# Kernel tuning notes

Measured on AMD Instinct MI355X. Metric: run time of the kernel, lower is better.

The kernel has to match this reference:

```python
import jax, jax.numpy as jnp
import numpy as np

P, V, GRID = 64, 6890, 32
V_SUB = 256          # vertex subsample for the SDF-grid proxy
SCALE_FACTOR = 0.2   # forward() default
SDF_BAND = 0.15      # proxy: phi = relu(band - dist_to_surface) >= 0
N_FACES = 13776


def _trilinear(vol, pts):
    """torch grid_sample 3D, mode=bilinear, padding=zeros, align_corners=False.
    vol: [D,H,W]; pts: [...,3] with (x,y,z) in [-1,1] mapping to (W,H,D)."""
    D, H, W = vol.shape
    x = ((pts[..., 0] + 1.0) * W - 1.0) * 0.5
    y = ((pts[..., 1] + 1.0) * H - 1.0) * 0.5
    z = ((pts[..., 2] + 1.0) * D - 1.0) * 0.5
    x0 = jnp.floor(x).astype(jnp.int32); fx = x - x0
    y0 = jnp.floor(y).astype(jnp.int32); fy = y - y0
    z0 = jnp.floor(z).astype(jnp.int32); fz = z - z0

    def corner(xi, yi, zi, w):
        inb = (xi >= 0) & (xi < W) & (yi >= 0) & (yi < H) & (zi >= 0) & (zi < D)
        v = vol[jnp.clip(zi, 0, D - 1), jnp.clip(yi, 0, H - 1), jnp.clip(xi, 0, W - 1)]
        return jnp.where(inb, v, 0.0) * w

    return (corner(x0,     y0,     z0,     (1 - fx) * (1 - fy) * (1 - fz))
          + corner(x0 + 1, y0,     z0,     fx       * (1 - fy) * (1 - fz))
          + corner(x0,     y0 + 1, z0,     (1 - fx) * fy       * (1 - fz))
          + corner(x0 + 1, y0 + 1, z0,     fx       * fy       * (1 - fz))
          + corner(x0,     y0,     z0 + 1, (1 - fx) * (1 - fy) * fz)
          + corner(x0 + 1, y0,     z0 + 1, fx       * (1 - fy) * fz)
          + corner(x0,     y0 + 1, z0 + 1, (1 - fx) * fy       * fz)
          + corner(x0 + 1, y0 + 1, z0 + 1, fx       * fy       * fz))


def _compute_phi(verts_cs):
    """Deterministic non-negative SDF-grid proxy (stands in for the external
    SDF CUDA op; original computes it under no_grad). verts_cs: [P,V,3] in [-1,1].
    Returns phi: [P,GRID,GRID,GRID] (D,H,W indexing)."""
    # cell centers in normalized coords (align_corners=False convention)
    lin = (2.0 * jnp.arange(GRID, dtype=verts_cs.dtype) + 1.0) / GRID - 1.0
    zz, yy, xx = jnp.meshgrid(lin, lin, lin, indexing='ij')
    gp = jnp.stack([xx, yy, zz], axis=-1).reshape(-1, 3)  # [G^3,3] (x,y,z)
    stride = V // V_SUB
    sub = verts_cs[:, ::stride, :][:, :V_SUB]             # [P,V_SUB,3]

    def per_person(v):  # v: [V_SUB,3]
        d2 = jnp.sum((gp[:, None, :] - v[None, :, :]) ** 2, axis=-1)  # [G^3,V_SUB]
        d = jnp.sqrt(jnp.min(d2, axis=-1))
        return jnp.maximum(SDF_BAND - d, 0.0).reshape(GRID, GRID, GRID)

    return jax.lax.map(per_person, sub)  # sequential over people: bounds peak memory


def _forward(vertices, translation):
    sg = jax.lax.stop_gradient
    verts = vertices + translation[:, None, :]                      # [P,V,3]
    n = verts.shape[0]
    bmin = sg(jnp.min(verts, axis=1))                               # [P,3] (no_grad bboxes)
    bmax = sg(jnp.max(verts, axis=1))
    # overlap(i,j) per axis: not (min_i > max_j or min_j > max_i)
    ov = jnp.all((bmin[:, None, :] <= bmax[None, :, :]) &
                 (bmin[None, :, :] <= bmax[:, None, :]), axis=-1)   # [P,P], diag True
    # faithful to original ~filter_isolated_boxes: kept only if overlapping ALL others
    valid = jnp.all(ov, axis=1)                                     # [P]
    nv = jnp.sum(valid.astype(verts.dtype))
    center = (bmin + bmax) * 0.5                                    # [P,3]
    scale = (1.0 + SCALE_FACTOR) * 0.5 * jnp.max(bmax - bmin, axis=-1)  # [P]
    verts_cs = sg((verts - center[:, None, :]) / scale[:, None, None])
    phi = sg(_compute_phi(verts_cs))                                # [P,G,G,G]
    # coordinates of ALL people's vertices in person-i's grid frame: [P,P,V,3]
    loc = (verts[None, :, :, :] - center[:, None, None, :]) / scale[:, None, None, None]
    phi_val = jax.vmap(_trilinear)(phi, loc.reshape(n, n * V, 3)).reshape(n, n, V)
    # pair (i,j) contributes iff both valid and i != j (weights[i]=0 in the loop)
    pair_w = (valid[:, None] & valid[None, :] & ~jnp.eye(n, dtype=bool)).astype(verts.dtype)
    denom = jnp.maximum(nv, 1.0) ** 2
    return jnp.sum(pair_w * jnp.sum(phi_val, axis=-1)) / denom


def setup_inputs() -> dict:
    key = jax.random.key(0)
    k1, k2, k3 = jax.random.split(key, 3)
    vertices = jax.random.normal(k1, (P, V, 3), dtype=jnp.float32) * 0.2
    translation = jax.random.uniform(k2, (P, 3), dtype=jnp.float32, minval=-0.3, maxval=0.3)
    faces = jax.random.randint(k3, (N_FACES, 3), 0, V, dtype=jnp.int32)
    return {"vertices": vertices, "translation": translation, "faces": faces}


def reference(vertices, translation, faces):
    # faces only feed the external SDF op (replaced by the phi proxy); unused here
    return _forward(vertices, translation)
```

## Files before the change

### kernel.cpp

```cpp
#include <hip/hip_runtime.h>


#define NP 64
#define NVERT 6890
#define NV3 (NVERT*3)
#define GRD 32
#define QDIM 34
#define QPLANE (QDIM*QDIM)
#define QVOL (QDIM*QPLANE)
#define VSUB 256
#define VSTRIDE 26
#define BAND 0.15f
#define PHI_SCALE 64.0f
#define INV_PHI_SCALE 0.015625f
#define LDS_BYTES (QVOL*2 + 64)
#define SAMPLE_BLOCKS (8*NP)

typedef float floatx2 __attribute__((ext_vector_type(2)));

__device__ __forceinline__ float wave_min(float v) {
  #pragma unroll
  for (int off = 32; off > 0; off >>= 1) v = fminf(v, __shfl_down(v, off));
  return v;
}
__device__ __forceinline__ float wave_max(float v) {
  #pragma unroll
  for (int off = 32; off > 0; off >>= 1) v = fmaxf(v, __shfl_down(v, off));
  return v;
}
__device__ __forceinline__ float wave_sum(float v) {
  #pragma unroll
  for (int off = 32; off > 0; off >>= 1) v += __shfl_down(v, off);
  return v;
}

__global__ __launch_bounds__(1024) void k_soa_bounds(
    const float* __restrict__ verts, const float* __restrict__ trans,
    float* __restrict__ vertsT, float* __restrict__ bbox,
    float* __restrict__ accp, unsigned int* __restrict__ donep) {
  int p = blockIdx.x;
  int tid = threadIdx.x;
  if (p == 0 && tid == 0) { accp[0] = 0.0f; donep[0] = 0u; }
  const float* vp = verts + (size_t)p * NV3;
  float tx = trans[p*3+0], ty = trans[p*3+1], tz = trans[p*3+2];
  float* o0 = vertsT + (size_t)(p*3+0) * NVERT;
  float* o1 = vertsT + (size_t)(p*3+1) * NVERT;
  float* o2 = vertsT + (size_t)(p*3+2) * NVERT;
  float mnx=1e30f, mny=1e30f, mnz=1e30f, mxx=-1e30f, mxy=-1e30f, mxz=-1e30f;
  for (int t2 = tid; t2 < NVERT/2; t2 += 1024) {
    const float* b = vp + t2*6;
    floatx2 A = *(const floatx2*)(b);
    floatx2 B = *(const floatx2*)(b+2);
    floatx2 C = *(const floatx2*)(b+4);
    mnx=fminf(mnx,fminf(A.x,B.y)); mxx=fmaxf(mxx,fmaxf(A.x,B.y));
    mny=fminf(mny,fminf(A.y,C.x)); mxy=fmaxf(mxy,fmaxf(A.y,C.x));
    mnz=fminf(mnz,fminf(B.x,C.y)); mxz=fmaxf(mxz,fmaxf(B.x,C.y));
    floatx2 sx = {A.x+tx, B.y+tx};
    floatx2 sy = {A.y+ty, C.x+ty};
    floatx2 sz = {B.x+tz, C.y+tz};
    *(floatx2*)(o0 + 2*t2) = sx;
    *(floatx2*)(o1 + 2*t2) = sy;
    *(floatx2*)(o2 + 2*t2) = sz;
  }
  mnx=wave_min(mnx)+tx; mny=wave_min(mny)+ty; mnz=wave_min(mnz)+tz;
  mxx=wave_max(mxx)+tx; mxy=wave_max(mxy)+ty; mxz=wave_max(mxz)+tz;
  __shared__ float s[16][6];
  int wave = tid >> 6, lane = tid & 63;
  if (lane == 0) {
    s[wave][0]=mnx; s[wave][1]=mny; s[wave][2]=mnz;
    s[wave][3]=mxx; s[wave][4]=mxy; s[wave][5]=mxz;
  }
  __syncthreads();
  if (tid == 0) {
    float a0=s[0][0],a1=s[0][1],a2=s[0][2],b0=s[0][3],b1=s[0][4],b2=s[0][5];
    for (int w = 1; w < 16; ++w) {
      a0=fminf(a0,s[w][0]); a1=fminf(a1,s[w][1]); a2=fminf(a2,s[w][2]);
      b0=fmaxf(b0,s[w][3]); b1=fmaxf(b1,s[w][4]); b2=fmaxf(b2,s[w][5]);
    }
    bbox[p*3+0]=a0; bbox[p*3+1]=a1; bbox[p*3+2]=a2;
    bbox[192+p*3+0]=b0; bbox[192+p*3+1]=b1; bbox[192+p*3+2]=b2;
  }
}

__global__ __launch_bounds__(1024) void k_phi(
    const float* __restrict__ verts, const float* __restrict__ trans,
    const float* __restrict__ bbox, unsigned short* __restrict__ pairs,
    float* __restrict__ centerg,
    float* __restrict__ validg, int* __restrict__ jlistg,
    int* __restrict__ jcountg, float* __restrict__ nvg) {
  int p = blockIdx.x >> 2;
  int zq = blockIdx.x & 3;
  int tid = threadIdx.x;
  int x = tid & 31, y = tid >> 5;

  __shared__ float kv[VSUB][3];
  __shared__ float phib[8][32][32];
  __shared__ int nkeep;

  const float inv = 1.0f / (float)GRD;
  if (tid == 0) nkeep = 0;
  __syncthreads();

  float bx0 = bbox[p*3+0], by0 = bbox[p*3+1], bz0 = bbox[p*3+2];
  float bx1 = bbox[192+p*3+0], by1 = bbox[192+p*3+1], bz1 = bbox[192+p*3+2];
  float cx = 0.5f*(bx0+bx1), cy = 0.5f*(by0+by1), cz = 0.5f*(bz0+bz1);
  float ext = fmaxf(bx1-bx0, fmaxf(by1-by0, bz1-bz0));
  float is = 1.0f / (0.6f * ext);

  if (zq == 0 && tid == 0) {
    centerg[p*4+0] = cx; centerg[p*4+1] = cy; centerg[p*4+2] = cz;
    centerg[p*4+3] = is * 16.0f;
  }
  if (blockIdx.x == 0 && tid < 64) {
    bool valid = true;
    for (int j = 0; j < NP; ++j) {
      bool ov = true;
      #pragma unroll
      for (int c = 0; c < 3; ++c)
        ov = ov && (bbox[tid*3+c] <= bbox[192+j*3+c]) &&
                   (bbox[j*3+c] <= bbox[192+tid*3+c]);
      valid = valid && ov;
    }
    unsigned long long mm = __ballot(valid);
    if (valid) {
      int pos = (int)__popcll(mm & ((1ull << tid) - 1ull));
      jlistg[pos] = tid;
    }
    validg[tid] = valid ? 1.0f : 0.0f;
    if (tid == 0) {
      jcountg[0] = (int)__popcll(mm);
      nvg[0] = (float)__popcll(mm);
    }
  }

  if (tid < VSUB) {
    int v = tid * VSTRIDE;
    const float* vp = verts + (size_t)p * NV3 + (size_t)v * 3;
    float X = (vp[0] + trans[p*3+0] - cx) * is;
    float Y = (vp[1] + trans[p*3+1] - cy) * is;
    float Z = (vp[2] + trans[p*3+2] - cz) * is;
    float zlo = (2.0f*(zq*8)     + 1.0f) * inv - 1.0f;
    float zhi = (2.0f*(zq*8 + 7) + 1.0f) * inv - 1.0f;
    float dz = fmaxf(fmaxf(zlo - Z, Z - zhi), 0.0f);
    if (dz < BAND) {
      int idx = atomicAdd(&nkeep, 1);
      kv[idx][0] = X; kv[idx][1] = Y; kv[idx][2] = Z;
    }
  }
  __syncthreads();
  int nk = nkeep;

  float gx = (2.0f*x + 1.0f) * inv - 1.0f;
  float gy = (2.0f*y + 1.0f) * inv - 1.0f;
  float gz[8];
  #pragma unroll
  for (int k = 0; k < 8; ++k) gz[k] = (2.0f*(zq*8+k) + 1.0f) * inv - 1.0f;

  float d2[8];
  #pragma unroll
  for (int k = 0; k < 8; ++k) d2[k] = 1e30f;

  int w = tid >> 6;
  float ylo = (4.0f*w + 1.0f) * inv - 1.0f;
  float yhi = (4.0f*w + 3.0f) * inv - 1.0f;

  for (int v = 0; v < nk; ++v) {
    float Y = kv[v][1];
    if (fmaxf(ylo - Y, Y - yhi) >= BAND) continue;
    float dx = gx - kv[v][0];
    float dy = gy - Y;
    float vz = kv[v][2];
    float r2 = fmaf(dy, dy, dx*dx);
    #pragma unroll
    for (int k = 0; k < 8; ++k) {
      float dz = gz[k] - vz;
      d2[k] = fminf(d2[k], fmaf(dz, dz, r2));
    }
  }
  #pragma unroll
  for (int k = 0; k < 8; ++k)
    phib[k][y][x] = fmaxf(BAND - sqrtf(d2[k]), 0.0f) * PHI_SCALE;
  __syncthreads();

  unsigned short* qp = pairs + (size_t)p * QVOL;
  for (int idx = tid; idx < QPLANE; idx += 1024) {
    int iy = idx / QDIM, ix = idx % QDIM;
    int gyy = iy - 1, gxx = ix - 1;
    bool gyok = (unsigned)gyy < 32u;
    bool aok = gyok && ((unsigned)gxx < 32u);
    bool bok = gyok && ((unsigned)ix  < 32u);
    int ya = gyok ? gyy : 0;
    int xa = aok ? gxx : 0;
    int xb = bok ? ix : 0;
    #pragma unroll
    for (int k = 0; k < 8; ++k) {
      float a = aok ? phib[k][ya][xa] : 0.0f;
      float b = bok ? phib[k][ya][xb] : 0.0f;
      int pk = __builtin_amdgcn_cvt_pk_fp8_f32(a, b, 0, false);
      qp[(zq*8 + k + 1)*QPLANE + idx] = (unsigned short)(pk & 0xffff);
    }
    if (zq == 0) qp[idx] = 0;
    if (zq == 3) qp[33*QPLANE + idx] = 0;
  }
}

__device__ __forceinline__ float qsample(const unsigned short* q,
                                         float X, float Y, float Z) {
  X = fminf(fmaxf(X, 0.0f), 33.99f);
  Y = fminf(fmaxf(Y, 0.0f), 32.999f);
  Z = fminf(fmaxf(Z, 0.0f), 32.999f);
  float xf = floorf(X), yf = floorf(Y), zf = floorf(Z);
  float fx = X - xf, fy = Y - yf, fz = Z - zf;
  int e = ((int)zf * QDIM + (int)yf) * QDIM + (int)xf;
  unsigned int w00 = q[e];
  unsigned int w10 = q[e + QDIM];
  unsigned int w01 = q[e + QPLANE];
  unsigned int w11 = q[e + QPLANE + QDIM];
  floatx2 c00 = __builtin_amdgcn_cvt_pk_f32_fp8((int)w00, false);
  floatx2 c10 = __builtin_amdgcn_cvt_pk_f32_fp8((int)w10, false);
  floatx2 c01 = __builtin_amdgcn_cvt_pk_f32_fp8((int)w01, false);
  floatx2 c11 = __builtin_amdgcn_cvt_pk_f32_fp8((int)w11, false);
  float u00 = fmaf(fx, c00.y - c00.x, c00.x);
  float u10 = fmaf(fx, c10.y - c10.x, c10.x);
  float u01 = fmaf(fx, c01.y - c01.x, c01.x);
  float u11 = fmaf(fx, c11.y - c11.x, c11.x);
  float a0 = fmaf(fy, u10 - u00, u00);
  float a1 = fmaf(fy, u11 - u01, u01);
  return fmaf(fz, a1 - a0, a0);
}

__global__ __launch_bounds__(896, 7) void k_sample(
    const float* __restrict__ vertsT, const float* __restrict__ centerg,
    const float* __restrict__ validg, const unsigned short* __restrict__ pairs,
    const int* __restrict__ jlistg, const int* __restrict__ jcountg,
    const float* __restrict__ nvg, float* __restrict__ accp,
    unsigned int* __restrict__ donep, float* __restrict__ out) {
  extern __shared__ unsigned char smem[];
  const unsigned short* sq = (const unsigned short*)smem;
  float* red = (float*)(smem + (size_t)QVOL * 2);

  int i = blockIdx.y;
  int tid = threadIdx.x;
  int njl = jcountg[0];

  if (validg[i] != 0.0f) {
    {
      const uint4* src = (const uint4*)(pairs + (size_t)i * QVOL);
      uint4* dst = (uint4*)smem;
      for (int t = tid; t < QVOL/8; t += 896) dst[t] = src[t];
    }
    __syncthreads();

    int v = blockIdx.x * 896 + tid;
    bool ok = v < NVERT;
    int vc = ok ? v : 0;
    float s16 = centerg[i*4+3];
    float bx = fmaf(-centerg[i*4+0], s16, 16.5f) + (ok ? 0.0f : 1e9f);
    float by = fmaf(-centerg[i*4+1], s16, 16.5f);
    float bz = fmaf(-centerg[i*4+2], s16, 16.5f);

    float acc = 0.0f;
    #pragma unroll 2
    for (int t = 0; t < njl; ++t) {
      int jj = jlistg[t];
      if (jj == i) continue;
      const float* p0 = vertsT + (size_t)(jj*3) * NVERT;
      float X = fmaf(p0[vc],         s16, bx);
      float Y = fmaf(p0[NVERT+vc],   s16, by);
      float Z = fmaf(p0[2*NVERT+vc], s16, bz);
      acc += qsample(sq, X, Y, Z);
    }

    acc = wave_sum(acc);
    int wv = tid >> 6, lane = tid & 63;
    if (lane == 0) red[wv] = acc;
    __syncthreads();
    if (tid == 0) {
      float tot = 0.0f;
      #pragma unroll
      for (int w = 0; w < 14; ++w) tot += red[w];
      atomicAdd(accp, tot * INV_PHI_SCALE);
    }
  }

  if (tid == 0) {
    __threadfence();
    unsigned int old = atomicAdd(donep, 1u);
    if (old == SAMPLE_BLOCKS - 1) {
      float nv = fmaxf(nvg[0], 1.0f);
      float loss = atomicAdd(accp, 0.0f);
      out[0] = loss / (nv * nv);
    }
  }
}

extern "C" void kernel_launch(void* const* d_in, const int* in_sizes, int n_in,
                              void* d_out, int out_size, void* d_ws, size_t ws_size,
                              hipStream_t stream) {
  const float* verts = (const float*)d_in[0];
  const float* trans = (const float*)d_in[1];
  float* out = (float*)d_out;

  unsigned short* pairs = (unsigned short*)d_ws;
  float* vertsT    = (float*)((unsigned char*)d_ws + (size_t)NP * QVOL * 2);
  float* bbox      = vertsT + (size_t)NP * NV3;
  float* centerg   = bbox + 384;
  float* validg    = centerg + NP*4;
  float* nvg       = validg + NP;
  float* accp      = nvg + 1;
  unsigned int* donep = (unsigned int*)(accp + 1);
  int* jlistg      = (int*)(donep + 1);
  int* jcountg     = jlistg + NP;

  hipFuncSetAttribute((const void*)k_sample,
                      hipFuncAttributeMaxDynamicSharedMemorySize, LDS_BYTES);

  k_soa_bounds<<<NP, 1024, 0, stream>>>(verts, trans, vertsT, bbox, accp, donep);
  k_phi<<<NP*4, 1024, 0, stream>>>(verts, trans, bbox, pairs, centerg,
                                   validg, jlistg, jcountg, nvg);
  k_sample<<<dim3(8, NP), 896, LDS_BYTES, stream>>>(vertsT, centerg, validg,
                                                    pairs, jlistg, jcountg,
                                                    nvg, accp, donep, out);
}
```

Before: 102.0 us.

## Counting-sort vertices by spatial cell before writing SoA buffer

The SoA transpose kernel now stages each person's translated vertices in LDS, buckets them into a 32x32 (z,y) cell histogram built with LDS atomics, prefix-scans it, and scatters vertices to global memory in bucket order. Since the final loss is a sum over vertices, reordering preserves the result. The intent is to make the later trilinear sampling kernel hit nearby phi voxels in neighbouring threads, improving LDS and cache locality. The cost is about 100KB of dynamic LDS per block, extra passes and syncs, and non-coalesced scattered global writes.

```diff
diff --git a/kernel.cpp b/kernel.cpp
--- a/kernel.cpp
+++ b/kernel.cpp
@@ -16,6 +16,14 @@
 #define LDS_BYTES (QVOL*2 + 64)
 #define SAMPLE_BLOCKS (8*NP)
 
+#define OFF_VX   0
+#define OFF_VY   27560
+#define OFF_VZ   55120
+#define OFF_KEY  82680
+#define OFF_HIST 96464
+#define OFF_RED  100560
+#define LDS_SOA  100960
+
 typedef float floatx2 __attribute__((ext_vector_type(2)));
 
 __device__ __forceinline__ float wave_min(float v) {
@@ -38,14 +46,20 @@
     const float* __restrict__ verts, const float* __restrict__ trans,
     float* __restrict__ vertsT, float* __restrict__ bbox,
     float* __restrict__ accp, unsigned int* __restrict__ donep) {
+  extern __shared__ unsigned char smem[];
+  float* vx = (float*)(smem + OFF_VX);
+  float* vy = (float*)(smem + OFF_VY);
+  float* vz = (float*)(smem + OFF_VZ);
+  unsigned short* keys = (unsigned short*)(smem + OFF_KEY);
+  int* hist = (int*)(smem + OFF_HIST);
+  float* s = (float*)(smem + OFF_RED);
+
   int p = blockIdx.x;
   int tid = threadIdx.x;
   if (p == 0 && tid == 0) { accp[0] = 0.0f; donep[0] = 0u; }
   const float* vp = verts + (size_t)p * NV3;
   float tx = trans[p*3+0], ty = trans[p*3+1], tz = trans[p*3+2];
-  float* o0 = vertsT + (size_t)(p*3+0) * NVERT;
-  float* o1 = vertsT + (size_t)(p*3+1) * NVERT;
-  float* o2 = vertsT + (size_t)(p*3+2) * NVERT;
+
   float mnx=1e30f, mny=1e30f, mnz=1e30f, mxx=-1e30f, mxy=-1e30f, mxz=-1e30f;
   for (int t2 = tid; t2 < NVERT/2; t2 += 1024) {
     const float* b = vp + t2*6;
@@ -55,30 +69,71 @@
     mnx=fminf(mnx,fminf(A.x,B.y)); mxx=fmaxf(mxx,fmaxf(A.x,B.y));
     mny=fminf(mny,fminf(A.y,C.x)); mxy=fmaxf(mxy,fmaxf(A.y,C.x));
     mnz=fminf(mnz,fminf(B.x,C.y)); mxz=fmaxf(mxz,fmaxf(B.x,C.y));
-    floatx2 sx = {A.x+tx, B.y+tx};
-    floatx2 sy = {A.y+ty, C.x+ty};
-    floatx2 sz = {B.x+tz, C.y+tz};
-    *(floatx2*)(o0 + 2*t2) = sx;
-    *(floatx2*)(o1 + 2*t2) = sy;
-    *(floatx2*)(o2 + 2*t2) = sz;
+    vx[2*t2] = A.x+tx; vx[2*t2+1] = B.y+tx;
+    vy[2*t2] = A.y+ty; vy[2*t2+1] = C.x+ty;
+    vz[2*t2] = B.x+tz; vz[2*t2+1] = C.y+tz;
   }
   mnx=wave_min(mnx)+tx; mny=wave_min(mny)+ty; mnz=wave_min(mnz)+tz;
   mxx=wave_max(mxx)+tx; mxy=wave_max(mxy)+ty; mxz=wave_max(mxz)+tz;
-  __shared__ float s[16][6];
   int wave = tid >> 6, lane = tid & 63;
   if (lane == 0) {
-    s[wave][0]=mnx; s[wave][1]=mny; s[wave][2]=mnz;
-    s[wave][3]=mxx; s[wave][4]=mxy; s[wave][5]=mxz;
-  }
+    s[wave*6+0]=mnx; s[wave*6+1]=mny; s[wave*6+2]=mnz;
+    s[wave*6+3]=mxx; s[wave*6+4]=mxy; s[wave*6+5]=mxz;
+  }
+  if (tid < 1024) hist[tid] = 0;
   __syncthreads();
   if (tid == 0) {
-    float a0=s[0][0],a1=s[0][1],a2=s[0][2],b0=s[0][3],b1=s[0][4],b2=s[0][5];
+    float a0=s[0],a1=s[1],a2=s[2],b0=s[3],b1=s[4],b2=s[5];
     for (int w = 1; w < 16; ++w) {
-      a0=fminf(a0,s[w][0]); a1=fminf(a1,s[w][1]); a2=fminf(a2,s[w][2]);
-      b0=fmaxf(b0,s[w][3]); b1=fmaxf(b1,s[w][4]); b2=fmaxf(b2,s[w][5]);
+      a0=fminf(a0,s[w*6+0]); a1=fminf(a1,s[w*6+1]); a2=fminf(a2,s[w*6+2]);
+      b0=fmaxf(b0,s[w*6+3]); b1=fmaxf(b1,s[w*6+4]); b2=fmaxf(b2,s[w*6+5]);
     }
     bbox[p*3+0]=a0; bbox[p*3+1]=a1; bbox[p*3+2]=a2;
     bbox[192+p*3+0]=b0; bbox[192+p*3+1]=b1; bbox[192+p*3+2]=b2;
+    s[0]=a0; s[1]=a1; s[2]=a2; s[3]=b0; s[4]=b1; s[5]=b2;
+  }
+  __syncthreads();
+  float cy = 0.5f*(s[1]+s[4]), cz = 0.5f*(s[2]+s[5]);
+  float ext = fmaxf(s[3]-s[0], fmaxf(s[4]-s[1], s[5]-s[2]));
+  float is16 = 16.0f / (0.6f * ext);
+
+  for (int v = tid; v < NVERT; v += 1024) {
+    float Yn = (vy[v] - cy) * is16 + 16.0f;
+    float Zn = (vz[v] - cz) * is16 + 16.0f;
+    int yc = (int)fminf(fmaxf(Yn, 0.0f), 31.0f);
+    int zc = (int)fminf(fmaxf(Zn, 0.0f), 31.0f);
+    int key = zc*32 + yc;
+    keys[v] = (unsigned short)key;
+    atomicAdd(&hist[key], 1);
+  }
+  __syncthreads();
+
+  if (tid < 64) {
+    int base = tid * 16;
+    int mysum = 0;
+    #pragma unroll
+    for (int k = 0; k < 16; ++k) mysum += hist[base+k];
+    int scan = mysum;
+    #pragma unroll
+    for (int off = 1; off < 64; off <<= 1) {
+      int n = __shfl_up(scan, off);
+      if (tid >= off) scan += n;
+    }
+    int run = scan - mysum;
+    #pragma unroll
+    for (int k = 0; k < 16; ++k) {
+      int old = hist[base+k]; hist[base+k] = run; run += old;
+    }
+  }
+  __syncthreads();
+
+  float* o0 = vertsT + (size_t)(p*3+0) * NVERT;
+  float* o1 = vertsT + (size_t)(p*3+1) * NVERT;
+  float* o2 = vertsT + (size_t)(p*3+2) * NVERT;
+  for (int v = tid; v < NVERT; v += 1024) {
+    int key = keys[v];
+    int dst = atomicAdd(&hist[key], 1);
+    o0[dst] = vx[v]; o1[dst] = vy[v]; o2[dst] = vz[v];
   }
 }
 
@@ -169,11 +224,11 @@
     if (fmaxf(ylo - Y, Y - yhi) >= BAND) continue;
     float dx = gx - kv[v][0];
     float dy = gy - Y;
-    float vz = kv[v][2];
+    float vzv = kv[v][2];
     float r2 = fmaf(dy, dy, dx*dx);
     #pragma unroll
     for (int k = 0; k < 8; ++k) {
-      float dz = gz[k] - vz;
+      float dz = gz[k] - vzv;
       d2[k] = fminf(d2[k], fmaf(dz, dz, r2));
     }
   }
@@ -312,10 +367,13 @@
   int* jlistg      = (int*)(donep + 1);
   int* jcountg     = jlistg + NP;
 
+  hipFuncSetAttribute((const void*)k_soa_bounds,
+                      hipFuncAttributeMaxDynamicSharedMemorySize, LDS_SOA);
   hipFuncSetAttribute((const void*)k_sample,
                       hipFuncAttributeMaxDynamicSharedMemorySize, LDS_BYTES);
 
-  k_soa_bounds<<<NP, 1024, 0, stream>>>(verts, trans, vertsT, bbox, accp, donep);
+  k_soa_bounds<<<NP, 1024, LDS_SOA, stream>>>(verts, trans, vertsT, bbox,
+                                              accp, donep);
   k_phi<<<NP*4, 1024, 0, stream>>>(verts, trans, bbox, pairs, centerg,
                                    validg, jlistg, jcountg, nvg);
   k_sample<<<dim3(8, NP), 896, LDS_BYTES, stream>>>(vertsT, centerg, validg,
```

After: 113.3 us. +11.1%, slower.
